# Kernel optimization log

Hardware: AMD Instinct MI355X
Metric: run time of the kernel (lower is better)

The kernel has to match this reference:

```python
import jax, jax.numpy as jnp
import numpy as np

N_NODES = 50000
N_EDGES = 800000
IN_CH = 64
OUT_CH = 64
HEADS = 4
NEG_SLOPE = 0.2  # PyG GATConv default


def setup_inputs() -> dict:
    key = jax.random.key(0)
    ks = jax.random.split(key, 8)
    x = jax.random.normal(ks[0], (N_NODES, IN_CH), dtype=jnp.float32)
    edge_index = jax.random.randint(ks[1], (2, N_EDGES), 0, N_NODES, dtype=jnp.int64)
    # GATConv params (concat=False): lin weight [in, H*out], att vectors [H, out], bias [out]
    W = jax.random.normal(ks[2], (IN_CH, HEADS * OUT_CH), dtype=jnp.float32) * (1.0 / np.sqrt(IN_CH))
    att_src = jax.random.normal(ks[3], (HEADS, OUT_CH), dtype=jnp.float32) * 0.1
    att_dst = jax.random.normal(ks[4], (HEADS, OUT_CH), dtype=jnp.float32) * 0.1
    bias = jnp.zeros((OUT_CH,), dtype=jnp.float32)
    fc_w = jax.random.normal(ks[5], (OUT_CH, 1), dtype=jnp.float32) * (1.0 / np.sqrt(OUT_CH))
    fc_b = jnp.zeros((1,), dtype=jnp.float32)
    return {"x": x, "edge_index": edge_index, "W": W, "att_src": att_src,
            "att_dst": att_dst, "bias": bias, "fc_w": fc_w, "fc_b": fc_b}


def reference(x, edge_index, W, att_src, att_dst, bias, fc_w, fc_b):
    N = x.shape[0]
    H, C = att_src.shape
    # per-node linear transform -> [N, H, C]
    xt = (x @ W).reshape(N, H, C)
    # PyG default add_self_loops=True
    loop = jnp.arange(N, dtype=edge_index.dtype)
    src = jnp.concatenate([edge_index[0], loop])  # message source j
    dst = jnp.concatenate([edge_index[1], loop])  # aggregation target i
    # attention logits: a_l . x_j + a_r . x_i, leaky_relu
    a_src = jnp.einsum('nhc,hc->nh', xt, att_src)  # [N, H]
    a_dst = jnp.einsum('nhc,hc->nh', xt, att_dst)
    e = jax.nn.leaky_relu(a_src[src] + a_dst[dst], NEG_SLOPE)  # [E, H]
    # segment softmax over incoming edges of each dst node
    m = jax.ops.segment_max(e, dst, num_segments=N)            # [N, H]
    e = jnp.exp(e - m[dst])
    s = jax.ops.segment_sum(e, dst, num_segments=N)            # [N, H]
    alpha = e / s[dst]                                          # [E, H]
    # weighted scatter-aggregate
    msg = xt[src] * alpha[:, :, None]                           # [E, H, C]
    out = jax.ops.segment_sum(msg, dst, num_segments=N)         # [N, H, C]
    out = out.mean(axis=1) + bias                               # concat=False -> mean heads
    h = jax.nn.relu(out)
    scores = (h @ fc_w + fc_b).squeeze(-1)                      # [N]
    return scores
```

## Files before the change

### kernel.cpp

```cpp
#include <hip/hip_runtime.h>
#include <hip/hip_bf16.h>

#define N_NODES 50000
#define N_EDGES 800000
#define HEADS   4
#define NEG_SLOPE 0.2f
#define SB      256
#define NB      ((N_NODES + SB - 1) / SB)
#define CAP     64
#define NT      ((N_NODES + 63) / 64)
#define NSC     782
#define EPB     512
#define INV_LN2 1.44269504088896340736f

typedef __attribute__((ext_vector_type(8))) _Float16 half8;
typedef __attribute__((ext_vector_type(4))) float f32x4;
typedef __attribute__((ext_vector_type(8))) unsigned short u16x8;

template <typename T> __device__ __forceinline__ float cvt(T v);
template <> __device__ __forceinline__ float cvt<float>(float v) { return v; }
template <> __device__ __forceinline__ float cvt<__hip_bfloat16>(__hip_bfloat16 v) {
    return __bfloat162float(v);
}
__device__ __forceinline__ unsigned short f2h(float f) {
    _Float16 h = (_Float16)f;
    return __builtin_bit_cast(unsigned short, h);
}
__device__ __forceinline__ float hbits(unsigned short u) {
    return (float)__builtin_bit_cast(_Float16, u);
}
__device__ __forceinline__ int probe_fp32(const unsigned* xw) {
    int sane = 0;
    for (int j = 0; j < 64; ++j) {
        unsigned e = (xw[j] >> 7) & 0xFF;
        sane += (e >= 90 && e <= 141);
    }
    return sane < 32;
}
__device__ __forceinline__ float loadW(int isf32, const void* W, int idx) {
    return isf32 ? ((const float*)W)[idx]
                 : cvt<__hip_bfloat16>(((const __hip_bfloat16*)W)[idx]);
}

template <typename T>
__device__ __forceinline__ void load8_f16(const T* p, _Float16* dst);
template <>
__device__ __forceinline__ void load8_f16<float>(const float* p, _Float16* dst) {
    float4 a = *(const float4*)p;
    float4 b = *(const float4*)(p + 4);
    dst[0] = (_Float16)a.x; dst[1] = (_Float16)a.y;
    dst[2] = (_Float16)a.z; dst[3] = (_Float16)a.w;
    dst[4] = (_Float16)b.x; dst[5] = (_Float16)b.y;
    dst[6] = (_Float16)b.z; dst[7] = (_Float16)b.w;
}
template <>
__device__ __forceinline__ void load8_f16<__hip_bfloat16>(const __hip_bfloat16* p,
                                                          _Float16* dst) {
    uint4 a = *(const uint4*)p;
    const unsigned short* u = (const unsigned short*)&a;
#pragma unroll
    for (int j = 0; j < 8; ++j)
        dst[j] = (_Float16)__uint_as_float(((unsigned)u[j]) << 16);
}

__global__ __launch_bounds__(256) void k_init(const unsigned* __restrict__ xw,
                                              const int* __restrict__ ei,
                                              const void* __restrict__ W,
                                              const void* __restrict__ att_src,
                                              const void* __restrict__ att_dst,
                                              int* __restrict__ cnt,
                                              int* __restrict__ flags,
                                              unsigned short* __restrict__ Batt,
                                              unsigned short* __restrict__ Bpost) {
    __shared__ float waS[256], waD[256];
    __shared__ int f32sh;
    if (blockIdx.x < NB) {
        int i = blockIdx.x * blockDim.x + threadIdx.x;
        if (i < N_NODES) cnt[i] = 0;
        if (blockIdx.x == 0 && threadIdx.x == 0) {
            int all0 = 1;
            for (int j = 1; j < 64; j += 2) all0 &= (ei[j] == 0);
            flags[0] = all0;
            flags[1] = probe_fp32(xw);
        }
        return;
    }
    const int pb = blockIdx.x - NB;
    if (threadIdx.x == 0) f32sh = probe_fp32(xw);
    __syncthreads();
    const int isf32 = f32sh;
    if (pb == 0) {
        int t = threadIdx.x, k = t >> 2, h = t & 3;
        float s = 0.f, d = 0.f;
        for (int c = 0; c < 64; ++c) {
            float w = loadW(isf32, W, k * 256 + h * 64 + c);
            float as = isf32 ? ((const float*)att_src)[h * 64 + c]
                             : cvt<__hip_bfloat16>(((const __hip_bfloat16*)att_src)[h * 64 + c]);
            float ad = isf32 ? ((const float*)att_dst)[h * 64 + c]
                             : cvt<__hip_bfloat16>(((const __hip_bfloat16*)att_dst)[h * 64 + c]);
            s = fmaf(w, as, s);
            d = fmaf(w, ad, d);
        }
        waS[t] = s * INV_LN2;
        waD[t] = d * INV_LN2;
        __syncthreads();
        if (threadIdx.x < 128) {
            int r = threadIdx.x;
            int q = (r >> 6) & 1, l = r & 63, n = l & 15;
            int kbase = q * 32 + ((l >> 4) & 3) * 8;
#pragma unroll
            for (int j = 0; j < 8; ++j) {
                int kk = kbase + j;
                float v = (n < 4) ? waS[kk * 4 + n]
                        : (n < 8) ? waD[kk * 4 + (n - 4)] : 0.f;
                Batt[r * 8 + j] = f2h(v);
            }
        }
    } else {
        const int sub = threadIdx.x >> 5, s = threadIdx.x & 31;
        const int t = (pb - 1) * 8 + sub;
        const int kt = t >> 2, nt = t & 3;
#pragma unroll
        for (int e = 0; e < 16; ++e) {
            int idx = s * 16 + e;
            int l = idx >> 3, j = idx & 7;
            int rs = kt * 32 + ((l >> 4) & 3) * 8 + j;
            int h = rs >> 6, k_in = rs & 63;
            int c = nt * 16 + (l & 15);
            Bpost[t * 512 + l * 8 + j] =
                f2h(loadW(isf32, W, k_in * 256 + h * 64 + c) * 0.25f);
        }
    }
}

template <typename T>
__device__ __forceinline__ void row_body(const T* __restrict__ x,
                                         const unsigned short* __restrict__ Batt,
                                         unsigned short* __restrict__ x16,
                                         float* __restrict__ a_src,
                                         float* __restrict__ a_dst) {
    const int tid = threadIdx.x;
    const int wav = tid >> 6, lane = tid & 63;
    const int quad = lane >> 4, r15 = lane & 15;
    const int m0 = blockIdx.x * 64;
    int gr = m0 + wav * 16 + r15;
    if (gr >= N_NODES) gr = N_NODES - 1;
    half8 afrag[2];
#pragma unroll
    for (int q = 0; q < 2; ++q) {
        _Float16 tmp[8];
        load8_f16<T>(x + (size_t)gr * 64 + q * 32 + quad * 8, tmp);
#pragma unroll
        for (int j = 0; j < 8; ++j) afrag[q][j] = tmp[j];
    }
    f32x4 acc = (f32x4){0.f, 0.f, 0.f, 0.f};
    const half8* bp = (const half8*)Batt;
    acc = __builtin_amdgcn_mfma_f32_16x16x32_f16(afrag[0], bp[lane], acc, 0, 0, 0);
    acc = __builtin_amdgcn_mfma_f32_16x16x32_f16(afrag[1], bp[64 + lane], acc, 0, 0, 0);
    if (r15 < 8) {
#pragma unroll
        for (int r = 0; r < 4; ++r) {
            int grow = m0 + wav * 16 + quad * 4 + r;
            if (grow < N_NODES) {
                if (r15 < 4) a_src[grow * HEADS + r15]       = acc[r];
                else         a_dst[grow * HEADS + (r15 - 4)] = acc[r];
            }
        }
    }
    {
        int row = m0 + (tid >> 2), seg = tid & 3;
        if (row < N_NODES) {
            _Float16 tmp[16];
            load8_f16<T>(x + (size_t)row * 64 + seg * 16, tmp);
            load8_f16<T>(x + (size_t)row * 64 + seg * 16 + 8, tmp + 8);
            *(u16x8*)(x16 + (size_t)row * 64 + seg * 16)     = *(const u16x8*)tmp;
            *(u16x8*)(x16 + (size_t)row * 64 + seg * 16 + 8) = *(const u16x8*)(tmp + 8);
        }
    }
}

__global__ __launch_bounds__(256) void k_mid(const void* __restrict__ x,
                                             const unsigned short* __restrict__ Batt,
                                             const int* __restrict__ ei,
                                             const int* __restrict__ flags,
                                             int* __restrict__ cnt,
                                             unsigned short* __restrict__ col_pad,
                                             unsigned short* __restrict__ x16,
                                             float* __restrict__ a_src,
                                             float* __restrict__ a_dst) {
    const int f64 = flags[0];
    const int base = blockIdx.x * EPB + threadIdx.x;
    int srcv[2], dstv[2], pos[2];
#pragma unroll
    for (int k = 0; k < 2; ++k) {
        int t = base + k * 256;
        if (t < N_EDGES) {
            if (f64) {
                int2 s2 = *(const int2*)(ei + 2 * t);
                int2 d2 = *(const int2*)(ei + 2 * N_EDGES + 2 * t);
                srcv[k] = s2.x; dstv[k] = d2.x;
            } else { srcv[k] = ei[t]; dstv[k] = ei[N_EDGES + t]; }
        } else dstv[k] = -1;
    }
#pragma unroll
    for (int k = 0; k < 2; ++k)
        if (dstv[k] >= 0) pos[k] = atomicAdd(cnt + dstv[k], 1);
    if (blockIdx.x < NT) {
        if (flags[1]) row_body<float>((const float*)x, Batt, x16, a_src, a_dst);
        else          row_body<__hip_bfloat16>((const __hip_bfloat16*)x, Batt,
                                               x16, a_src, a_dst);
    }
#pragma unroll
    for (int k = 0; k < 2; ++k)
        if (dstv[k] >= 0 && pos[k] < CAP)
            col_pad[dstv[k] * CAP + pos[k]] = (unsigned short)srcv[k];
}

__global__ __launch_bounds__(256) void k_aggregate(const int* __restrict__ cnt,
                                                   const unsigned short* __restrict__ col_pad,
                                                   const float* __restrict__ a_src,
                                                   const float* __restrict__ a_dst,
                                                   const unsigned short* __restrict__ x16,
                                                   unsigned short* __restrict__ s_cat) {
    __shared__ __align__(16) int cS[4][64];
    __shared__ float4 peS[4][64];
    const int tid = threadIdx.x;
    const int wav = tid >> 6, lane = tid & 63;
    const int hlf = lane >> 5, l5 = lane & 31;
    const int wid = (blockIdx.x * blockDim.x + tid) >> 6;
    if (wid >= N_NODES) return;
    int* cSw = cS[wav];
    float4* peSw = peS[wav];
    int n = cnt[wid]; n = n > (CAP - 1) ? (CAP - 1) : n;
    const float4 ad = ((const float4*)a_dst)[wid];
    int mycol = wid;
    if (lane < n) mycol = (int)col_pad[wid * CAP + lane];
    const float4 as = ((const float4*)a_src)[mycol];
    float e0 = as.x + ad.x, e1 = as.y + ad.y;
    float e2 = as.z + ad.z, e3 = as.w + ad.w;
    e0 = e0 > 0.f ? e0 : NEG_SLOPE * e0;  e1 = e1 > 0.f ? e1 : NEG_SLOPE * e1;
    e2 = e2 > 0.f ? e2 : NEG_SLOPE * e2;  e3 = e3 > 0.f ? e3 : NEG_SLOPE * e3;
    float4 pe = make_float4(exp2f(e0), exp2f(e1), exp2f(e2), exp2f(e3));
    if (lane > n) pe = make_float4(0.f, 0.f, 0.f, 0.f);
    const int slot = (lane & 1) * 32 + (lane >> 1);
    cSw[slot] = mycol << 7;
    peS[wav][slot] = pe;
    const char* xb = (const char*)x16 + l5 * 4;
    float a0 = 0.f, a1 = 0.f, a2 = 0.f, a3 = 0.f;
    float a4 = 0.f, a5 = 0.f, a6 = 0.f, a7 = 0.f;
    const int nr = (n + 2) >> 1;
    const int*    cB = cSw + hlf * 32;
    const float4* pB = peSw + hlf * 32;
#define ACC2(D, P) { float x0 = hbits((unsigned short)((D) & 0xffff)); \
                     float x1 = hbits((unsigned short)((D) >> 16)); \
                     a0 = fmaf((P).x, x0, a0); a1 = fmaf((P).x, x1, a1); \
                     a2 = fmaf((P).y, x0, a2); a3 = fmaf((P).y, x1, a3); \
                     a4 = fmaf((P).z, x0, a4); a5 = fmaf((P).z, x1, a5); \
                     a6 = fmaf((P).w, x0, a6); a7 = fmaf((P).w, x1, a7); }
    int r = 0;
    for (; r + 4 <= nr; r += 4) {
        const int4 cc = *(const int4*)(cB + r);
        unsigned dA = *(const unsigned*)(xb + cc.x);
        unsigned dB = *(const unsigned*)(xb + cc.y);
        unsigned dC = *(const unsigned*)(xb + cc.z);
        unsigned dD = *(const unsigned*)(xb + cc.w);
        float4 pA = pB[r], pBv = pB[r + 1], pC = pB[r + 2], pD = pB[r + 3];
        ACC2(dA, pA); ACC2(dB, pBv); ACC2(dC, pC); ACC2(dD, pD);
    }
    for (; r < nr; ++r) {
        int c = cB[r];
        unsigned d = *(const unsigned*)(xb + c);
        float4 p = pB[r];
        ACC2(d, p);
    }
#undef ACC2
    a0 += __shfl_xor(a0, 32, 64); a1 += __shfl_xor(a1, 32, 64);
    a2 += __shfl_xor(a2, 32, 64); a3 += __shfl_xor(a3, 32, 64);
    a4 += __shfl_xor(a4, 32, 64); a5 += __shfl_xor(a5, 32, 64);
    a6 += __shfl_xor(a6, 32, 64); a7 += __shfl_xor(a7, 32, 64);
    float sp0 = pe.x, sp1 = pe.y, sp2 = pe.z, sp3 = pe.w;
#pragma unroll
    for (int off = 32; off > 0; off >>= 1) {
        sp0 += __shfl_xor(sp0, off, 64);
        sp1 += __shfl_xor(sp1, off, 64);
        sp2 += __shfl_xor(sp2, off, 64);
        sp3 += __shfl_xor(sp3, off, 64);
    }
    const float r0 = 1.f / sp0, r1 = 1.f / sp1;
    const float r2 = 1.f / sp2, r3 = 1.f / sp3;
    unsigned short* sr = s_cat + (size_t)wid * 256 + 2 * l5;
    unsigned w0 = (unsigned)f2h(a0 * r0) | ((unsigned)f2h(a1 * r0) << 16);
    unsigned w1 = (unsigned)f2h(a2 * r1) | ((unsigned)f2h(a3 * r1) << 16);
    unsigned w2 = (unsigned)f2h(a4 * r2) | ((unsigned)f2h(a5 * r2) << 16);
    unsigned w3 = (unsigned)f2h(a6 * r3) | ((unsigned)f2h(a7 * r3) << 16);
    *(unsigned*)(sr)       = w0;
    *(unsigned*)(sr + 64)  = w1;
    *(unsigned*)(sr + 128) = w2;
    *(unsigned*)(sr + 192) = w3;
}

template <typename T>
__device__ __forceinline__ void post_body(const unsigned short* __restrict__ s_cat,
                                          const unsigned short* __restrict__ Bpost,
                                          const T* __restrict__ bias,
                                          const T* __restrict__ fc_w,
                                          const T* __restrict__ fc_b,
                                          float* __restrict__ out) {
    const int tid = threadIdx.x;
    const int wav = tid >> 6, lane = tid & 63;
    const int quad = lane >> 4, r15 = lane & 15;
    const int m0 = blockIdx.x * 64;
    int gr = m0 + wav * 16 + r15;
    if (gr >= N_NODES) gr = N_NODES - 1;
    const half8* arow = (const half8*)((const char*)s_cat + (size_t)gr * 512);
    half8 af[8];
#pragma unroll
    for (int kt = 0; kt < 8; ++kt) af[kt] = arow[kt * 4 + quad];
    f32x4 acc[4];
#pragma unroll
    for (int nt = 0; nt < 4; ++nt) acc[nt] = (f32x4){0.f, 0.f, 0.f, 0.f};
    const half8* bp = (const half8*)Bpost;
#pragma unroll
    for (int kt = 0; kt < 8; ++kt)
#pragma unroll
        for (int nt = 0; nt < 4; ++nt)
            acc[nt] = __builtin_amdgcn_mfma_f32_16x16x32_f16(
                af[kt], bp[(kt * 4 + nt) * 64 + lane], acc[nt], 0, 0, 0);
    float bi[4], fw[4];
#pragma unroll
    for (int nt = 0; nt < 4; ++nt) {
        int c = nt * 16 + r15;
        bi[nt] = cvt<T>(bias[c]);
        fw[nt] = cvt<T>(fc_w[c]);
    }
    const float fcb = cvt<T>(fc_b[0]);
#pragma unroll
    for (int r = 0; r < 4; ++r) {
        float p = 0.f;
#pragma unroll
        for (int nt = 0; nt < 4; ++nt) {
            float o = acc[nt][r] + bi[nt];
            o = o > 0.f ? o : 0.f;
            p = fmaf(o, fw[nt], p);
        }
#pragma unroll
        for (int off = 8; off > 0; off >>= 1) p += __shfl_xor(p, off, 64);
        int row = m0 + wav * 16 + quad * 4 + r;
        if (r15 == 0 && row < N_NODES) out[row] = p + fcb;
    }
}

__global__ __launch_bounds__(256) void k_post(const unsigned short* __restrict__ s_cat,
                                              const unsigned short* __restrict__ Bpost,
                                              const void* __restrict__ bias,
                                              const void* __restrict__ fc_w,
                                              const void* __restrict__ fc_b,
                                              const int* __restrict__ flags,
                                              float* __restrict__ out) {
    if (flags[1])
        post_body<float>(s_cat, Bpost, (const float*)bias, (const float*)fc_w,
                         (const float*)fc_b, out);
    else
        post_body<__hip_bfloat16>(s_cat, Bpost, (const __hip_bfloat16*)bias,
                                  (const __hip_bfloat16*)fc_w,
                                  (const __hip_bfloat16*)fc_b, out);
}

extern "C" void kernel_launch(void* const* d_in, const int* in_sizes, int n_in,
                              void* d_out, int out_size, void* d_ws, size_t ws_size,
                              hipStream_t stream) {
    const void* x       = d_in[0];
    const int*  ei      = (const int*)d_in[1];
    const void* W       = d_in[2];
    const void* att_src = d_in[3];
    const void* att_dst = d_in[4];
    const void* bias    = d_in[5];
    const void* fc_w    = d_in[6];
    const void* fc_b    = d_in[7];
    float* out = (float*)d_out;

    char* wsb = (char*)d_ws;
    unsigned short* x16   = (unsigned short*)wsb;
    unsigned short* s_cat = (unsigned short*)(wsb + 6400000);
    unsigned short* Batt  = (unsigned short*)(wsb + 32000000);
    unsigned short* Bpost = (unsigned short*)(wsb + 32002048);
    float* a_src = (float*)(wsb + 32034816);
    float* a_dst = (float*)(wsb + 32834816);
    unsigned short* col_pad = (unsigned short*)(wsb + 33634816);
    int* cnt   = (int*)(wsb + 40034816);
    int* flags = (int*)(wsb + 40234816);

    k_init<<<NB + 5, 256, 0, stream>>>((const unsigned*)x, ei, W, att_src,
                                       att_dst, cnt, flags, Batt, Bpost);
    k_mid<<<NT + NSC, 256, 0, stream>>>(x, Batt, ei, flags, cnt, col_pad,
                                        x16, a_src, a_dst);
    k_aggregate<<<((size_t)N_NODES * 64 + 255) / 256, 256, 0, stream>>>(
        cnt, col_pad, a_src, a_dst, x16, s_cat);
    k_post<<<NT, 256, 0, stream>>>(s_cat, Bpost, bias, fc_w, fc_b, flags, out);
}
```

Measured before the change: 179.2 us.

## Replace global per-node atomics with two-level region bucketing for CSR build

Edge-to-CSR construction now first bins edges into 98 destination regions of 512 nodes using shared-memory histograms and one global atomic per region per block. It writes packed (src,dst) records into per-region queues, and a new scatter kernel builds the padded column lists and counts with shared atomics. This removes the per-node global cnt zeroing and the scattered global atomics, at the cost of an extra kernel launch, an intermediate queue pass, and a capped queue size (QCAP) that could drop edges for skewed inputs. Separately, the aggregate kernel now sums softmax denominators inside the accumulation loop, which replaces a full wave shuffle reduction with a single half-swap.

Result: faster. 174.4 us (-2.7%).

```diff
diff --git a/kernel.cpp b/kernel.cpp
--- a/kernel.cpp
+++ b/kernel.cpp
@@ -5,12 +5,12 @@
 #define N_EDGES 800000
 #define HEADS   4
 #define NEG_SLOPE 0.2f
-#define SB      256
-#define NB      ((N_NODES + SB - 1) / SB)
 #define CAP     64
 #define NT      ((N_NODES + 63) / 64)
-#define NSC     782
-#define EPB     512
+#define EPB     2048
+#define NEB     ((N_EDGES + EPB - 1) / EPB)
+#define NREG    98
+#define QCAP    9216
 #define INV_LN2 1.44269504088896340736f
 
 typedef __attribute__((ext_vector_type(8))) _Float16 half8;
@@ -68,16 +68,15 @@
                                               const void* __restrict__ W,
                                               const void* __restrict__ att_src,
                                               const void* __restrict__ att_dst,
-                                              int* __restrict__ cnt,
+                                              int* __restrict__ qcnt,
                                               int* __restrict__ flags,
                                               unsigned short* __restrict__ Batt,
                                               unsigned short* __restrict__ Bpost) {
     __shared__ float waS[256], waD[256];
     __shared__ int f32sh;
-    if (blockIdx.x < NB) {
-        int i = blockIdx.x * blockDim.x + threadIdx.x;
-        if (i < N_NODES) cnt[i] = 0;
-        if (blockIdx.x == 0 && threadIdx.x == 0) {
+    if (blockIdx.x == 0) {
+        if (threadIdx.x < NREG) qcnt[threadIdx.x] = 0;
+        if (threadIdx.x == 0) {
             int all0 = 1;
             for (int j = 1; j < 64; j += 2) all0 &= (ei[j] == 0);
             flags[0] = all0;
@@ -85,7 +84,7 @@
         }
         return;
     }
-    const int pb = blockIdx.x - NB;
+    const int pb = blockIdx.x - 1;
     if (threadIdx.x == 0) f32sh = probe_fp32(xw);
     __syncthreads();
     const int isf32 = f32sh;
@@ -183,37 +182,82 @@
                                              const unsigned short* __restrict__ Batt,
                                              const int* __restrict__ ei,
                                              const int* __restrict__ flags,
-                                             int* __restrict__ cnt,
-                                             unsigned short* __restrict__ col_pad,
+                                             int* __restrict__ qcnt,
+                                             unsigned* __restrict__ queue,
                                              unsigned short* __restrict__ x16,
                                              float* __restrict__ a_src,
                                              float* __restrict__ a_dst) {
-    const int f64 = flags[0];
-    const int base = blockIdx.x * EPB + threadIdx.x;
-    int srcv[2], dstv[2], pos[2];
-#pragma unroll
-    for (int k = 0; k < 2; ++k) {
-        int t = base + k * 256;
-        if (t < N_EDGES) {
-            if (f64) {
-                int2 s2 = *(const int2*)(ei + 2 * t);
-                int2 d2 = *(const int2*)(ei + 2 * N_EDGES + 2 * t);
-                srcv[k] = s2.x; dstv[k] = d2.x;
-            } else { srcv[k] = ei[t]; dstv[k] = ei[N_EDGES + t]; }
-        } else dstv[k] = -1;
-    }
-#pragma unroll
-    for (int k = 0; k < 2; ++k)
-        if (dstv[k] >= 0) pos[k] = atomicAdd(cnt + dstv[k], 1);
-    if (blockIdx.x < NT) {
-        if (flags[1]) row_body<float>((const float*)x, Batt, x16, a_src, a_dst);
-        else          row_body<__hip_bfloat16>((const __hip_bfloat16*)x, Batt,
-                                               x16, a_src, a_dst);
-    }
-#pragma unroll
-    for (int k = 0; k < 2; ++k)
-        if (dstv[k] >= 0 && pos[k] < CAP)
-            col_pad[dstv[k] * CAP + pos[k]] = (unsigned short)srcv[k];
+    __shared__ int hist[NREG];
+    __shared__ int qbaseS[NREG];
+    const int tid = threadIdx.x;
+    const bool edge_blk = ((blockIdx.x & 1) == 0);
+    const int eb = blockIdx.x >> 1;
+    unsigned rec[8]; int reg[8], lpos[8];
+    int histv = 0, mybase = 0;
+    if (edge_blk) {
+        if (tid < NREG) hist[tid] = 0;
+        __syncthreads();
+        const int f64 = flags[0];
+        const int base = eb * EPB + tid;
+#pragma unroll
+        for (int k = 0; k < 8; ++k) {
+            int t = base + k * 256;
+            if (t < N_EDGES) {
+                int s, d;
+                if (f64) { s = ei[2 * t]; d = ei[2 * N_EDGES + 2 * t]; }
+                else     { s = ei[t];     d = ei[N_EDGES + t]; }
+                reg[k] = d >> 9;
+                rec[k] = (unsigned)s | ((unsigned)d << 16);
+            } else reg[k] = -1;
+        }
+#pragma unroll
+        for (int k = 0; k < 8; ++k)
+            if (reg[k] >= 0) lpos[k] = atomicAdd(&hist[reg[k]], 1);
+        __syncthreads();
+        if (tid < NREG) {
+            histv = hist[tid];
+            if (histv) mybase = atomicAdd(qcnt + tid, histv);
+        }
+    }
+    if (flags[1]) row_body<float>((const float*)x, Batt, x16, a_src, a_dst);
+    else          row_body<__hip_bfloat16>((const __hip_bfloat16*)x, Batt,
+                                           x16, a_src, a_dst);
+    if (edge_blk) {
+        if (tid < NREG) qbaseS[tid] = mybase;
+        __syncthreads();
+#pragma unroll
+        for (int k = 0; k < 8; ++k)
+            if (reg[k] >= 0) {
+                int o = qbaseS[reg[k]] + lpos[k];
+                if (o < QCAP)
+                    queue[(size_t)reg[k] * QCAP + o] = rec[k];
+            }
+    }
+}
+
+__global__ __launch_bounds__(256) void k_scat(const unsigned* __restrict__ queue,
+                                              const int* __restrict__ qcnt,
+                                              unsigned short* __restrict__ col_pad,
+                                              int* __restrict__ cnt) {
+    __shared__ int cl[512];
+    const int b = blockIdx.x, tid = threadIdx.x;
+    const int base = b << 9;
+    cl[tid] = 0; cl[tid + 256] = 0;
+    __syncthreads();
+    int m = qcnt[b]; m = m > QCAP ? QCAP : m;
+    const unsigned* q = queue + (size_t)b * QCAP;
+#pragma unroll 4
+    for (int i = tid; i < m; i += 256) {
+        unsigned rec = q[i];
+        int d = rec >> 16, s = rec & 0xffff;
+        int p = atomicAdd(&cl[d - base], 1);
+        if (p < CAP) col_pad[(size_t)d * CAP + p] = (unsigned short)s;
+    }
+    __syncthreads();
+    int j = base + tid;
+    if (j < N_NODES) cnt[j] = cl[tid];
+    j += 256;
+    if (j < N_NODES) cnt[j] = cl[tid + 256];
 }
 
 __global__ __launch_bounds__(256) void k_aggregate(const int* __restrict__ cnt,
@@ -248,6 +292,7 @@
     const char* xb = (const char*)x16 + l5 * 4;
     float a0 = 0.f, a1 = 0.f, a2 = 0.f, a3 = 0.f;
     float a4 = 0.f, a5 = 0.f, a6 = 0.f, a7 = 0.f;
+    float sp0 = 0.f, sp1 = 0.f, sp2 = 0.f, sp3 = 0.f;
     const int nr = (n + 2) >> 1;
     const int*    cB = cSw + hlf * 32;
     const float4* pB = peSw + hlf * 32;
@@ -256,7 +301,8 @@
                      a0 = fmaf((P).x, x0, a0); a1 = fmaf((P).x, x1, a1); \
                      a2 = fmaf((P).y, x0, a2); a3 = fmaf((P).y, x1, a3); \
                      a4 = fmaf((P).z, x0, a4); a5 = fmaf((P).z, x1, a5); \
-                     a6 = fmaf((P).w, x0, a6); a7 = fmaf((P).w, x1, a7); }
+                     a6 = fmaf((P).w, x0, a6); a7 = fmaf((P).w, x1, a7); \
+                     sp0 += (P).x; sp1 += (P).y; sp2 += (P).z; sp3 += (P).w; }
     int r = 0;
     for (; r + 4 <= nr; r += 4) {
         const int4 cc = *(const int4*)(cB + r);
@@ -278,14 +324,8 @@
     a2 += __shfl_xor(a2, 32, 64); a3 += __shfl_xor(a3, 32, 64);
     a4 += __shfl_xor(a4, 32, 64); a5 += __shfl_xor(a5, 32, 64);
     a6 += __shfl_xor(a6, 32, 64); a7 += __shfl_xor(a7, 32, 64);
-    float sp0 = pe.x, sp1 = pe.y, sp2 = pe.z, sp3 = pe.w;
-#pragma unroll
-    for (int off = 32; off > 0; off >>= 1) {
-        sp0 += __shfl_xor(sp0, off, 64);
-        sp1 += __shfl_xor(sp1, off, 64);
-        sp2 += __shfl_xor(sp2, off, 64);
-        sp3 += __shfl_xor(sp3, off, 64);
-    }
+    sp0 += __shfl_xor(sp0, 32, 64); sp1 += __shfl_xor(sp1, 32, 64);
+    sp2 += __shfl_xor(sp2, 32, 64); sp3 += __shfl_xor(sp3, 32, 64);
     const float r0 = 1.f / sp0, r1 = 1.f / sp1;
     const float r2 = 1.f / sp2, r3 = 1.f / sp3;
     unsigned short* sr = s_cat + (size_t)wid * 256 + 2 * l5;
@@ -382,6 +422,7 @@
     char* wsb = (char*)d_ws;
     unsigned short* x16   = (unsigned short*)wsb;
     unsigned short* s_cat = (unsigned short*)(wsb + 6400000);
+    unsigned* queue = (unsigned*)s_cat;
     unsigned short* Batt  = (unsigned short*)(wsb + 32000000);
     unsigned short* Bpost = (unsigned short*)(wsb + 32002048);
     float* a_src = (float*)(wsb + 32034816);
@@ -389,11 +430,13 @@
     unsigned short* col_pad = (unsigned short*)(wsb + 33634816);
     int* cnt   = (int*)(wsb + 40034816);
     int* flags = (int*)(wsb + 40234816);
-
-    k_init<<<NB + 5, 256, 0, stream>>>((const unsigned*)x, ei, W, att_src,
-                                       att_dst, cnt, flags, Batt, Bpost);
-    k_mid<<<NT + NSC, 256, 0, stream>>>(x, Batt, ei, flags, cnt, col_pad,
-                                        x16, a_src, a_dst);
+    int* qcnt  = (int*)(wsb + 40234824);
+
+    k_init<<<6, 256, 0, stream>>>((const unsigned*)x, ei, W, att_src,
+                                  att_dst, qcnt, flags, Batt, Bpost);
+    k_mid<<<NT, 256, 0, stream>>>(x, Batt, ei, flags, qcnt, queue,
+                                  x16, a_src, a_dst);
+    k_scat<<<NREG, 256, 0, stream>>>(queue, qcnt, col_pad, cnt);
     k_aggregate<<<((size_t)N_NODES * 64 + 255) / 256, 256, 0, stream>>>(
         cnt, col_pad, a_src, a_dst, x16, s_cat);
     k_post<<<NT, 256, 0, stream>>>(s_cat, Bpost, bias, fc_w, fc_b, flags, out);
```
